# Kernel tuning notes

Measured on AMD Instinct MI355X. Metric: run time of the kernel, lower is better.

## Reference

```python
import jax, jax.numpy as jnp
import numpy as np
import math

EMB_DIM = 1024
N_HEADS = 16
HEAD_DIM = EMB_DIM // N_HEADS
B, T = 4, 2048


def bitlinear(x, w):
    # BitNet b1.58 absmean ternary quantization. NOTE: the source never
    # rescales the ternary weights by `scale`, so forward uses raw {-1,0,1}.
    scale = jnp.maximum(jnp.mean(jnp.abs(w)), 1e-8)
    w_ternary = jnp.clip(jnp.round(w / scale), -1.0, 1.0)
    w_q = w + jax.lax.stop_gradient(w_ternary - w)  # STE
    return x @ w_q.T


def setup_inputs() -> dict:
    key = jax.random.key(0)
    k1, k2, k3 = jax.random.split(key, 3)
    x = jax.random.normal(k1, (B, T, EMB_DIM), dtype=jnp.float32)
    w_qkv = jax.random.normal(k2, (3 * EMB_DIM, EMB_DIM), dtype=jnp.float32) * 0.02
    w_out = jax.random.normal(k3, (EMB_DIM, EMB_DIM), dtype=jnp.float32) * 0.02
    return {"x": x, "w_qkv": w_qkv, "w_out": w_out}


def reference(x, w_qkv, w_out):
    Bc, Tc, C = x.shape
    qkv = bitlinear(x, w_qkv)  # [B, T, 3C]
    q, k, v = jnp.split(qkv, 3, axis=2)

    def split_heads(t):  # [B, T, C] -> [B, H, T, D]
        return t.reshape(Bc, Tc, N_HEADS, HEAD_DIM).transpose(0, 2, 1, 3)

    q, k, v = split_heads(q), split_heads(k), split_heads(v)
    scale = math.sqrt(HEAD_DIM)
    scores = jnp.einsum("bhqd,bhkd->bhqk", q, k) / scale  # [B, H, T, T]
    causal = jnp.triu(jnp.ones((Tc, Tc), dtype=bool), k=1)
    scores = jnp.where(causal, -jnp.inf, scores)
    attn = jax.nn.softmax(scores, axis=-1)
    out = jnp.einsum("bhqk,bhkd->bhqd", attn, v)  # [B, H, T, D]
    out = out.transpose(0, 2, 1, 3).reshape(Bc, Tc, C)
    return bitlinear(out, w_out)
```

## Files before the change

kernel.cpp:

```cpp
#include <hip/hip_runtime.h>
#include <hip/hip_bf16.h>

#define EMB   1024
#define NHEAD 16
#define HDIM  64
#define BSZ   4
#define SEQ   2048
#define MROWS (BSZ*SEQ)
#define NQKV  (3*EMB)

typedef __bf16 bf16;
typedef __bf16 bf16v8 __attribute__((ext_vector_type(8)));
typedef float  f32v4  __attribute__((ext_vector_type(4)));
typedef int    i32v4  __attribute__((ext_vector_type(4)));

#define MFMA16(a,b,c)  __builtin_amdgcn_mfma_f32_16x16x32_bf16((a),(b),(c),0,0,0)
#define MFMAI8(a,b,c)  __builtin_amdgcn_mfma_i32_16x16x64_i8((a),(b),(c),0,0,0)

__device__ __forceinline__ void gload_lds16(const void* g, void* l) {
  __builtin_amdgcn_global_load_lds((const __attribute__((address_space(1))) void*)g,
                                   (__attribute__((address_space(3))) void*)l,
                                   16, 0, 0);
}


__global__ void zero2_kernel(float* p) { p[threadIdx.x] = 0.f; }

__global__ void abs_sum_kernel(const float* __restrict__ w, int n, float* out) {
  float s = 0.f;
  for (int i = blockIdx.x * blockDim.x + threadIdx.x; i < n; i += gridDim.x * blockDim.x)
    s += fabsf(w[i]);
  #pragma unroll
  for (int off = 32; off; off >>= 1) s += __shfl_down(s, off, 64);
  __shared__ float red[4];
  int lane = threadIdx.x & 63, wid = threadIdx.x >> 6;
  if (lane == 0) red[wid] = s;
  __syncthreads();
  if (threadIdx.x == 0) atomicAdd(out, red[0] + red[1] + red[2] + red[3]);
}

__global__ void ternarize_i8_kernel(const float* __restrict__ w, int n,
                                    const float* __restrict__ sum, char* __restrict__ out) {
  int i = blockIdx.x * blockDim.x + threadIdx.x;
  if (i >= n) return;
  float scale = fmaxf(*sum / (float)n, 1e-8f);
  float t = rintf(w[i] / scale);
  t = fmaxf(-1.f, fminf(1.f, t));
  out[i] = (char)(int)t;
}

__global__ void ternarize_bf16_kernel(const float* __restrict__ w, int n,
                                      const float* __restrict__ sum, bf16* __restrict__ out) {
  int i = blockIdx.x * blockDim.x + threadIdx.x;
  if (i >= n) return;
  float scale = fmaxf(*sum / (float)n, 1e-8f);
  float t = rintf(w[i] / scale);
  t = fmaxf(-1.f, fminf(1.f, t));
  out[i] = (bf16)t;
}

__global__ void quant_x_kernel(const float* __restrict__ x, char* __restrict__ p1,
                               char* __restrict__ p2, int n) {
  int i = blockIdx.x * blockDim.x + threadIdx.x;
  if (i >= n) return;
  float v = x[i];
  float q1 = fminf(fmaxf(rintf(v * 16.f), -127.f), 127.f);
  float r = v - q1 * 0.0625f;
  float q2 = fminf(fmaxf(rintf(r * 4096.f), -127.f), 127.f);
  p1[i] = (char)(int)q1;
  p2[i] = (char)(int)q2;
}


__launch_bounds__(256, 2)
__global__ void gemm_qkv_kernel(const char* __restrict__ xq1, const char* __restrict__ xq2,
                                const char* __restrict__ w8,
                                bf16* __restrict__ qh, bf16* __restrict__ ql,
                                bf16* __restrict__ kh, bf16* __restrict__ kl,
                                bf16* __restrict__ vv) {
  __shared__ __align__(16) char A1[128 * 64];
  __shared__ __align__(16) char A2[128 * 64];
  __shared__ __align__(16) char Bs[128 * 64];
  const int tid = threadIdx.x;
  const int lane = tid & 63, wid = tid >> 6;
  const int quad = lane >> 4, l16 = lane & 15;
  const int m0 = blockIdx.x * 128, n0 = blockIdx.y * 128;
  const int wm = (wid >> 1) * 64, wn = (wid & 1) * 64;
  const int asw = (l16 >> 1) & 3;
  i32v4 acc1[4][4] = {};
  i32v4 acc2[4][4] = {};

  for (int kt = 0; kt < EMB / 64; ++kt) {
    __syncthreads();
    #pragma unroll
    for (int r = 0; r < 2; ++r) {
      int li = r * 256 + tid;
      int row = li >> 2, cs = li & 3;
      int cg = cs ^ ((row >> 1) & 3);
      gload_lds16(xq1 + (size_t)(m0 + row) * EMB + kt * 64 + cg * 16, &A1[li * 16]);
      gload_lds16(xq2 + (size_t)(m0 + row) * EMB + kt * 64 + cg * 16, &A2[li * 16]);
      gload_lds16(w8  + (size_t)(n0 + row) * EMB + kt * 64 + cg * 16, &Bs[li * 16]);
    }
    __syncthreads();
    i32v4 af1[4], af2[4], bfr[4];
    #pragma unroll
    for (int i = 0; i < 4; ++i) {
      int arow = wm + i * 16 + l16;
      int off = arow * 64 + ((quad ^ asw) * 16);
      af1[i] = *(const i32v4*)&A1[off];
      af2[i] = *(const i32v4*)&A2[off];
      int brow = wn + i * 16 + l16;
      bfr[i] = *(const i32v4*)&Bs[brow * 64 + ((quad ^ asw) * 16)];
    }
    #pragma unroll
    for (int i = 0; i < 4; ++i)
      #pragma unroll
      for (int j = 0; j < 4; ++j) {
        acc1[i][j] = MFMAI8(af1[i], bfr[j], acc1[i][j]);
        acc2[i][j] = MFMAI8(af2[i], bfr[j], acc2[i][j]);
      }
  }
  const float S1 = 0.0625f, S2 = 1.f / 4096.f;
  const float QSCALE = 0.18033688011112042f;
  #pragma unroll
  for (int i = 0; i < 4; ++i)
    #pragma unroll
    for (int j = 0; j < 4; ++j)
      #pragma unroll
      for (int r = 0; r < 4; ++r) {
        int m = m0 + wm + i * 16 + quad * 4 + r;
        int n = n0 + wn + j * 16 + l16;
        float c = (float)acc1[i][j][r] * S1 + (float)acc2[i][j][r] * S2;
        int b = m >> 11, t = m & (SEQ - 1);
        int region = n >> 10, c1 = n & 1023, h = c1 >> 6, d = c1 & 63;
        size_t idx = (((size_t)(b * NHEAD + h) * SEQ + t) << 6) + d;
        if (region == 0)      { float cs = c * QSCALE; bf16 hi = (bf16)cs; qh[idx] = hi; ql[idx] = (bf16)(cs - (float)hi); }
        else if (region == 1) { bf16 hi = (bf16)c; kh[idx] = hi; kl[idx] = (bf16)(c - (float)hi); }
        else                  { vv[idx] = (bf16)c; }
      }
}


__global__ void transpose_v_kernel(const bf16* __restrict__ v, bf16* __restrict__ vt) {
  __shared__ bf16 tile[64 * 72];
  const int tid = threadIdx.x;
  const int bh = blockIdx.y, t0 = blockIdx.x * 64;
  const size_t base = (size_t)bh * SEQ * HDIM;
  #pragma unroll
  for (int r = 0; r < 2; ++r) {
    int li = r * 256 + tid;
    int row = li >> 3, col = (li & 7) * 8;
    bf16v8 val = *(const bf16v8*)(v + base + (size_t)(t0 + row) * HDIM + col);
    #pragma unroll
    for (int j = 0; j < 8; ++j) tile[(col + j) * 72 + row] = val[j];
  }
  __syncthreads();
  #pragma unroll
  for (int r = 0; r < 2; ++r) {
    int li = r * 256 + tid;
    int drow = li >> 3, tcol = (li & 7) * 8;
    bf16v8 val;
    #pragma unroll
    for (int j = 0; j < 8; ++j) val[j] = tile[drow * 72 + tcol + j];
    *(bf16v8*)(vt + base + (size_t)drow * SEQ + t0 + tcol) = val;
  }
}


__launch_bounds__(512, 4)
__global__ void attn_kernel(const bf16* __restrict__ qh, const bf16* __restrict__ ql,
                            const bf16* __restrict__ kh, const bf16* __restrict__ kl,
                            const bf16* __restrict__ vt, bf16* __restrict__ o) {
  __shared__ __align__(16) char smem[66560];
  bf16* Qh = (bf16*)smem;
  bf16* Ql = (bf16*)(smem + 16384);
  bf16* Pw = (bf16*)(smem + 49152);
  const int tid = threadIdx.x;
  const int lane = tid & 63, wid = tid >> 6;
  const int quad = lane >> 4, l16 = lane & 15;
  const int xs = l16 & 7;
  const int pair = blockIdx.x;
  const int bh = blockIdx.y;
  const size_t base = (size_t)bh * SEQ * HDIM;

  const int srow = tid >> 3, scg = (tid & 7) ^ (srow & 7);
  auto stage_kv = [&](char* dst, int k0) {
    gload_lds16(kh + base + (size_t)(k0 + srow) * HDIM + scg * 8, (bf16*)dst + (size_t)tid * 8);
    gload_lds16(kl + base + (size_t)(k0 + srow) * HDIM + scg * 8, (bf16*)(dst + 8192) + (size_t)tid * 8);
    gload_lds16(vt + base + (size_t)srow * SEQ + k0 + scg * 8,    (bf16*)(dst + 16384) + (size_t)tid * 8);
  };

  bf16v8 ones_f;
  {
    bf16 v1 = (l16 == 0) ? (bf16)1.0f : (bf16)0.0f;
    #pragma unroll
    for (int j = 0; j < 8; ++j) ones_f[j] = v1;
  }
  const int b = bh >> 4, h = bh & 15;

  for (int phase = 0; phase < 2; ++phase) {
    const int qt = phase ? (7 - pair) : (8 + pair);
    const int q0 = qt * 128;

    __syncthreads();
    #pragma unroll
    for (int r = 0; r < 2; ++r) {
      int li = r * 512 + tid;
      int row = li >> 3, cg = (li & 7) ^ (row & 7);
      gload_lds16(qh + base + (size_t)(q0 + row) * HDIM + cg * 8, &Qh[li * 8]);
      gload_lds16(ql + base + (size_t)(q0 + row) * HDIM + cg * 8, &Ql[li * 8]);
    }
    __syncthreads();
    bf16v8 qhf[2], qlf[2];
    #pragma unroll
    for (int kk = 0; kk < 2; ++kk) {
      int off = (wid * 16 + l16) * 64 + (((kk << 2) | quad) ^ xs) * 8;
      qhf[kk] = *(const bf16v8*)&Qh[off];
      qlf[kk] = *(const bf16v8*)&Ql[off];
    }
    __syncthreads();

    f32v4 oacc[4] = {};
    f32v4 lacc = {};
    float mrow[4];
    #pragma unroll
    for (int r = 0; r < 4; ++r) mrow[r] = -1e30f;

    const int qrow_hi = q0 + wid * 16 + 15;
    const int ntiles = 2 * qt + 2;

    stage_kv(smem, 0);

    for (int ktile = 0; ktile < ntiles; ++ktile) {
      char* cb = smem + (size_t)((ktile & 1) * 24576);
      char* nb = smem + (size_t)(((ktile + 1) & 1) * 24576);
      __syncthreads();
      if (ktile + 1 < ntiles) stage_kv(nb, (ktile + 1) * 64);
      const int k0 = ktile * 64;
      if (k0 > qrow_hi) continue;

      bf16* Kh_ = (bf16*)cb;
      bf16* Kl_ = (bf16*)(cb + 8192);
      bf16* Vt_ = (bf16*)(cb + 16384);

      f32v4 sacc[4] = {};
      #pragma unroll
      for (int kk = 0; kk < 2; ++kk) {
        const int co = (((kk << 2) | quad) ^ xs) * 8;
        bf16v8 khf[4], klf[4];
        #pragma unroll
        for (int nt = 0; nt < 4; ++nt) {
          khf[nt] = *(const bf16v8*)&Kh_[(nt * 16 + l16) * 64 + co];
          klf[nt] = *(const bf16v8*)&Kl_[(nt * 16 + l16) * 64 + co];
        }
        #pragma unroll
        for (int nt = 0; nt < 4; ++nt) {
          sacc[nt] = MFMA16(qhf[kk], khf[nt], sacc[nt]);
          sacc[nt] = MFMA16(qhf[kk], klf[nt], sacc[nt]);
          sacc[nt] = MFMA16(qlf[kk], khf[nt], sacc[nt]);
        }
      }

      const int qrow_base = q0 + wid * 16 + quad * 4;
      #pragma unroll
      for (int nt = 0; nt < 4; ++nt) {
        int key = k0 + nt * 16 + l16;
        #pragma unroll
        for (int r = 0; r < 4; ++r)
          if (key > qrow_base + r) sacc[nt][r] = -1e30f;
      }
      float mnew[4], alpha[4];
      #pragma unroll
      for (int r = 0; r < 4; ++r) {
        float mx = fmaxf(fmaxf(sacc[0][r], sacc[1][r]), fmaxf(sacc[2][r], sacc[3][r]));
        #pragma unroll
        for (int off = 8; off; off >>= 1) mx = fmaxf(mx, __shfl_xor(mx, off, 64));
        mnew[r] = fmaxf(mrow[r], mx);
        alpha[r] = __builtin_amdgcn_exp2f(mrow[r] - mnew[r]);
        mrow[r] = mnew[r];
      }
      bf16* pwave = Pw + wid * (16 * 68);
      #pragma unroll
      for (int nt = 0; nt < 4; ++nt)
        #pragma unroll
        for (int r = 0; r < 4; ++r)
          pwave[(quad * 4 + r) * 68 + nt * 16 + l16] =
              (bf16)__builtin_amdgcn_exp2f(sacc[nt][r] - mnew[r]);
      #pragma unroll
      for (int r = 0; r < 4; ++r) {
        lacc[r] *= alpha[r];
        #pragma unroll
        for (int dt = 0; dt < 4; ++dt) oacc[dt][r] *= alpha[r];
      }

      #pragma unroll
      for (int kk = 0; kk < 2; ++kk) {
        bf16v8 pf = *(const bf16v8*)&pwave[l16 * 68 + kk * 32 + quad * 8];
        const int co = (((kk << 2) | quad) ^ xs) * 8;
        lacc = MFMA16(pf, ones_f, lacc);
        #pragma unroll
        for (int dt = 0; dt < 4; ++dt) {
          bf16v8 vf = *(const bf16v8*)&Vt_[(dt * 16 + l16) * 64 + co];
          oacc[dt] = MFMA16(pf, vf, oacc[dt]);
        }
      }
    }

    float lrow[4];
    #pragma unroll
    for (int r = 0; r < 4; ++r) lrow[r] = __shfl(lacc[r], lane & 48, 64);

    #pragma unroll
    for (int dt = 0; dt < 4; ++dt)
      #pragma unroll
      for (int r = 0; r < 4; ++r) {
        int q = q0 + wid * 16 + quad * 4 + r;
        int d = dt * 16 + l16;
        float val = oacc[dt][r] / lrow[r];
        o[((size_t)(b * SEQ + q)) * EMB + h * HDIM + d] = (bf16)val;
      }
  }
}


__launch_bounds__(256, 2)
__global__ void gemm_out_kernel(const bf16* __restrict__ oin, const bf16* __restrict__ wt,
                                float* __restrict__ out) {
  __shared__ __align__(16) bf16 As_[128 * 64];
  __shared__ __align__(16) bf16 Bs_[128 * 64];
  const int tid = threadIdx.x;
  const int lane = tid & 63, wid = tid >> 6;
  const int quad = lane >> 4, l16 = lane & 15;
  const int m0 = blockIdx.x * 128, n0 = blockIdx.y * 128;
  const int wm = (wid >> 1) * 64, wn = (wid & 1) * 64;
  f32v4 acc[4][4] = {};

  for (int kt = 0; kt < EMB / 64; ++kt) {
    __syncthreads();
    #pragma unroll
    for (int r = 0; r < 4; ++r) {
      int li = r * 256 + tid;
      int row = li >> 3, col = (li & 7) * 8;
      gload_lds16(oin + (size_t)(m0 + row) * EMB + kt * 64 + col, &As_[li * 8]);
      gload_lds16(wt  + (size_t)(n0 + row) * EMB + kt * 64 + col, &Bs_[li * 8]);
    }
    __syncthreads();
    #pragma unroll
    for (int kk = 0; kk < 2; ++kk) {
      bf16v8 af[4], bfr[4];
      #pragma unroll
      for (int i = 0; i < 4; ++i) {
        af[i]  = *(const bf16v8*)&As_[(wm + i * 16 + l16) * 64 + kk * 32 + quad * 8];
        bfr[i] = *(const bf16v8*)&Bs_[(wn + i * 16 + l16) * 64 + kk * 32 + quad * 8];
      }
      #pragma unroll
      for (int i = 0; i < 4; ++i)
        #pragma unroll
        for (int j = 0; j < 4; ++j)
          acc[i][j] = MFMA16(af[i], bfr[j], acc[i][j]);
    }
  }
  #pragma unroll
  for (int i = 0; i < 4; ++i)
    #pragma unroll
    for (int j = 0; j < 4; ++j)
      #pragma unroll
      for (int r = 0; r < 4; ++r) {
        int m = m0 + wm + i * 16 + quad * 4 + r;
        int n = n0 + wn + j * 16 + l16;
        out[(size_t)m * EMB + n] = acc[i][j][r];
      }
}


extern "C" void kernel_launch(void* const* d_in, const int* in_sizes, int n_in,
                              void* d_out, int out_size, void* d_ws, size_t ws_size,
                              hipStream_t stream) {
  const float* x     = (const float*)d_in[0];
  const float* w_qkv = (const float*)d_in[1];
  const float* w_out = (const float*)d_in[2];
  float* out = (float*)d_out;
  char* ws = (char*)d_ws;

  const size_t SZ  = (size_t)MROWS * EMB * sizeof(bf16);
  const size_t SZ8 = (size_t)MROWS * EMB;
  size_t off = 0;
  float* sums = (float*)ws;            off = 256;
  char*  wq8  = (char*)(ws + off);     off += (size_t)NQKV * EMB;
  bf16*  wo_t = (bf16*)(ws + off);     off += (size_t)EMB * EMB * sizeof(bf16);
  char*  xq1  = (char*)(ws + off);     off += SZ8;
  char*  xq2  = (char*)(ws + off);     off += SZ8;
  bf16*  qh   = (bf16*)(ws + off);     off += SZ;
  bf16*  ql   = (bf16*)(ws + off);     off += SZ;
  bf16*  kh   = (bf16*)(ws + off);     off += SZ;
  bf16*  kl   = (bf16*)(ws + off);     off += SZ;
  bf16*  vv   = (bf16*)(ws + off);     off += SZ;
  bf16*  vt   = (bf16*)xq1;
  bf16*  ob   = vv;
  (void)in_sizes; (void)n_in; (void)out_size; (void)ws_size;

  zero2_kernel<<<1, 2, 0, stream>>>(sums);
  abs_sum_kernel<<<256, 256, 0, stream>>>(w_qkv, NQKV * EMB, &sums[0]);
  abs_sum_kernel<<<256, 256, 0, stream>>>(w_out, EMB * EMB, &sums[1]);
  ternarize_i8_kernel<<<(NQKV * EMB) / 256, 256, 0, stream>>>(w_qkv, NQKV * EMB, &sums[0], wq8);
  ternarize_bf16_kernel<<<(EMB * EMB) / 256, 256, 0, stream>>>(w_out, EMB * EMB, &sums[1], wo_t);
  quant_x_kernel<<<(MROWS * EMB) / 256, 256, 0, stream>>>(x, xq1, xq2, MROWS * EMB);
  gemm_qkv_kernel<<<dim3(MROWS / 128, NQKV / 128), 256, 0, stream>>>(xq1, xq2, wq8, qh, ql, kh, kl, vv);
  transpose_v_kernel<<<dim3(SEQ / 64, BSZ * NHEAD), 256, 0, stream>>>(vv, vt);
  attn_kernel<<<dim3(8, BSZ * NHEAD), 512, 0, stream>>>(qh, ql, kh, kl, vt, ob);
  gemm_out_kernel<<<dim3(MROWS / 128, EMB / 128), 256, 0, stream>>>(ob, wo_t, out);
}
```

Before: 355.1 us.

## Give each attention wave 32 query rows to reuse K/V fragments

Attention blocks drop from 512 to 256 threads, and each wave now handles two 16-row query sub-tiles instead of one. K and V fragments loaded from LDS are therefore shared across twice as many MFMAs, halving LDS fragment reads per query row. The row-max reduction uses DPP row-shift ops instead of __shfl_xor. The costs are more registers per wave and fewer waves per block to hide latency. Some score MFMAs are also computed for fully masked sub-tiles.

```diff
diff --git a/kernel.cpp b/kernel.cpp
--- a/kernel.cpp
+++ b/kernel.cpp
@@ -22,6 +22,10 @@
                                    (__attribute__((address_space(3))) void*)l,
                                    16, 0, 0);
 }
+
+#define DPP_FMAX(x, ctrl) do {                                                     \
+    int _t = __builtin_amdgcn_update_dpp(0, __float_as_int(x), (ctrl), 0xf, 0xf, true); \
+    (x) = fmaxf((x), __int_as_float(_t)); } while (0)
 
 
 __global__ void zero2_kernel(float* p) { p[threadIdx.x] = 0.f; }
@@ -167,7 +171,7 @@
 }
 
 
-__launch_bounds__(512, 4)
+__launch_bounds__(256, 2)
 __global__ void attn_kernel(const bf16* __restrict__ qh, const bf16* __restrict__ ql,
                             const bf16* __restrict__ kh, const bf16* __restrict__ kl,
                             const bf16* __restrict__ vt, bf16* __restrict__ o) {
@@ -183,11 +187,15 @@
   const int bh = blockIdx.y;
   const size_t base = (size_t)bh * SEQ * HDIM;
 
-  const int srow = tid >> 3, scg = (tid & 7) ^ (srow & 7);
   auto stage_kv = [&](char* dst, int k0) {
-    gload_lds16(kh + base + (size_t)(k0 + srow) * HDIM + scg * 8, (bf16*)dst + (size_t)tid * 8);
-    gload_lds16(kl + base + (size_t)(k0 + srow) * HDIM + scg * 8, (bf16*)(dst + 8192) + (size_t)tid * 8);
-    gload_lds16(vt + base + (size_t)srow * SEQ + k0 + scg * 8,    (bf16*)(dst + 16384) + (size_t)tid * 8);
+    #pragma unroll
+    for (int r = 0; r < 2; ++r) {
+      int li = r * 256 + tid;
+      int srow = li >> 3, scg = (li & 7) ^ (srow & 7);
+      gload_lds16(kh + base + (size_t)(k0 + srow) * HDIM + scg * 8, (bf16*)dst + (size_t)li * 8);
+      gload_lds16(kl + base + (size_t)(k0 + srow) * HDIM + scg * 8, (bf16*)(dst + 8192) + (size_t)li * 8);
+      gload_lds16(vt + base + (size_t)srow * SEQ + k0 + scg * 8,    (bf16*)(dst + 16384) + (size_t)li * 8);
+    }
   };
 
   bf16v8 ones_f;
@@ -204,29 +212,34 @@
 
     __syncthreads();
     #pragma unroll
-    for (int r = 0; r < 2; ++r) {
-      int li = r * 512 + tid;
+    for (int r = 0; r < 4; ++r) {
+      int li = r * 256 + tid;
       int row = li >> 3, cg = (li & 7) ^ (row & 7);
       gload_lds16(qh + base + (size_t)(q0 + row) * HDIM + cg * 8, &Qh[li * 8]);
       gload_lds16(ql + base + (size_t)(q0 + row) * HDIM + cg * 8, &Ql[li * 8]);
     }
     __syncthreads();
-    bf16v8 qhf[2], qlf[2];
-    #pragma unroll
-    for (int kk = 0; kk < 2; ++kk) {
-      int off = (wid * 16 + l16) * 64 + (((kk << 2) | quad) ^ xs) * 8;
-      qhf[kk] = *(const bf16v8*)&Qh[off];
-      qlf[kk] = *(const bf16v8*)&Ql[off];
-    }
-    __syncthreads();
-
-    f32v4 oacc[4] = {};
-    f32v4 lacc = {};
-    float mrow[4];
-    #pragma unroll
-    for (int r = 0; r < 4; ++r) mrow[r] = -1e30f;
-
-    const int qrow_hi = q0 + wid * 16 + 15;
+    bf16v8 qhf[2][2], qlf[2][2];
+    #pragma unroll
+    for (int sub = 0; sub < 2; ++sub)
+      #pragma unroll
+      for (int kk = 0; kk < 2; ++kk) {
+        int off = (wid * 32 + sub * 16 + l16) * 64 + (((kk << 2) | quad) ^ xs) * 8;
+        qhf[sub][kk] = *(const bf16v8*)&Qh[off];
+        qlf[sub][kk] = *(const bf16v8*)&Ql[off];
+      }
+    __syncthreads();
+
+    f32v4 oacc[2][4] = {};
+    f32v4 lacc[2] = {};
+    float mrow[2][4];
+    #pragma unroll
+    for (int s = 0; s < 2; ++s)
+      #pragma unroll
+      for (int r = 0; r < 4; ++r) mrow[s][r] = -1e30f;
+
+    const int qw0 = q0 + wid * 32;
+    const int qrow_hi = qw0 + 31;
     const int ntiles = 2 * qt + 2;
 
     stage_kv(smem, 0);
@@ -243,7 +256,7 @@
       bf16* Kl_ = (bf16*)(cb + 8192);
       bf16* Vt_ = (bf16*)(cb + 16384);
 
-      f32v4 sacc[4] = {};
+      f32v4 sacc[2][4] = {};
       #pragma unroll
       for (int kk = 0; kk < 2; ++kk) {
         const int co = (((kk << 2) | quad) ^ xs) * 8;
@@ -254,71 +267,88 @@
           klf[nt] = *(const bf16v8*)&Kl_[(nt * 16 + l16) * 64 + co];
         }
         #pragma unroll
+        for (int sub = 0; sub < 2; ++sub)
+          #pragma unroll
+          for (int nt = 0; nt < 4; ++nt) {
+            sacc[sub][nt] = MFMA16(qhf[sub][kk], khf[nt], sacc[sub][nt]);
+            sacc[sub][nt] = MFMA16(qhf[sub][kk], klf[nt], sacc[sub][nt]);
+            sacc[sub][nt] = MFMA16(qlf[sub][kk], khf[nt], sacc[sub][nt]);
+          }
+      }
+
+      #pragma unroll
+      for (int sub = 0; sub < 2; ++sub) {
+        if (k0 > qw0 + sub * 16 + 15) continue;
+        const int qrow_base = qw0 + sub * 16 + quad * 4;
+        #pragma unroll
         for (int nt = 0; nt < 4; ++nt) {
-          sacc[nt] = MFMA16(qhf[kk], khf[nt], sacc[nt]);
-          sacc[nt] = MFMA16(qhf[kk], klf[nt], sacc[nt]);
-          sacc[nt] = MFMA16(qlf[kk], khf[nt], sacc[nt]);
-        }
-      }
-
-      const int qrow_base = q0 + wid * 16 + quad * 4;
-      #pragma unroll
-      for (int nt = 0; nt < 4; ++nt) {
-        int key = k0 + nt * 16 + l16;
-        #pragma unroll
-        for (int r = 0; r < 4; ++r)
-          if (key > qrow_base + r) sacc[nt][r] = -1e30f;
-      }
-      float mnew[4], alpha[4];
-      #pragma unroll
-      for (int r = 0; r < 4; ++r) {
-        float mx = fmaxf(fmaxf(sacc[0][r], sacc[1][r]), fmaxf(sacc[2][r], sacc[3][r]));
-        #pragma unroll
-        for (int off = 8; off; off >>= 1) mx = fmaxf(mx, __shfl_xor(mx, off, 64));
-        mnew[r] = fmaxf(mrow[r], mx);
-        alpha[r] = __builtin_amdgcn_exp2f(mrow[r] - mnew[r]);
-        mrow[r] = mnew[r];
-      }
-      bf16* pwave = Pw + wid * (16 * 68);
-      #pragma unroll
-      for (int nt = 0; nt < 4; ++nt)
-        #pragma unroll
-        for (int r = 0; r < 4; ++r)
-          pwave[(quad * 4 + r) * 68 + nt * 16 + l16] =
-              (bf16)__builtin_amdgcn_exp2f(sacc[nt][r] - mnew[r]);
-      #pragma unroll
-      for (int r = 0; r < 4; ++r) {
-        lacc[r] *= alpha[r];
-        #pragma unroll
-        for (int dt = 0; dt < 4; ++dt) oacc[dt][r] *= alpha[r];
+          int key = k0 + nt * 16 + l16;
+          #pragma unroll
+          for (int r = 0; r < 4; ++r)
+            if (key > qrow_base + r) sacc[sub][nt][r] = -1e30f;
+        }
+        float alpha[4];
+        #pragma unroll
+        for (int r = 0; r < 4; ++r) {
+          float mx = fmaxf(fmaxf(sacc[sub][0][r], sacc[sub][1][r]),
+                           fmaxf(sacc[sub][2][r], sacc[sub][3][r]));
+          DPP_FMAX(mx, 0x128);
+          DPP_FMAX(mx, 0x124);
+          DPP_FMAX(mx, 0x122);
+          DPP_FMAX(mx, 0x121);
+          float mnew = fmaxf(mrow[sub][r], mx);
+          alpha[r] = __builtin_amdgcn_exp2f(mrow[sub][r] - mnew);
+          mrow[sub][r] = mnew;
+        }
+        bf16* pwave = Pw + (wid * 2 + sub) * (16 * 68);
+        #pragma unroll
+        for (int nt = 0; nt < 4; ++nt)
+          #pragma unroll
+          for (int r = 0; r < 4; ++r)
+            pwave[(quad * 4 + r) * 68 + nt * 16 + l16] =
+                (bf16)__builtin_amdgcn_exp2f(sacc[sub][nt][r] - mrow[sub][r]);
+        #pragma unroll
+        for (int r = 0; r < 4; ++r) {
+          lacc[sub][r] *= alpha[r];
+          #pragma unroll
+          for (int dt = 0; dt < 4; ++dt) oacc[sub][dt][r] *= alpha[r];
+        }
       }
 
       #pragma unroll
       for (int kk = 0; kk < 2; ++kk) {
-        bf16v8 pf = *(const bf16v8*)&pwave[l16 * 68 + kk * 32 + quad * 8];
         const int co = (((kk << 2) | quad) ^ xs) * 8;
-        lacc = MFMA16(pf, ones_f, lacc);
-        #pragma unroll
-        for (int dt = 0; dt < 4; ++dt) {
-          bf16v8 vf = *(const bf16v8*)&Vt_[(dt * 16 + l16) * 64 + co];
-          oacc[dt] = MFMA16(pf, vf, oacc[dt]);
-        }
-      }
-    }
-
-    float lrow[4];
-    #pragma unroll
-    for (int r = 0; r < 4; ++r) lrow[r] = __shfl(lacc[r], lane & 48, 64);
-
-    #pragma unroll
-    for (int dt = 0; dt < 4; ++dt)
-      #pragma unroll
-      for (int r = 0; r < 4; ++r) {
-        int q = q0 + wid * 16 + quad * 4 + r;
-        int d = dt * 16 + l16;
-        float val = oacc[dt][r] / lrow[r];
-        o[((size_t)(b * SEQ + q)) * EMB + h * HDIM + d] = (bf16)val;
-      }
+        bf16v8 vf[4];
+        #pragma unroll
+        for (int dt = 0; dt < 4; ++dt)
+          vf[dt] = *(const bf16v8*)&Vt_[(dt * 16 + l16) * 64 + co];
+        #pragma unroll
+        for (int sub = 0; sub < 2; ++sub) {
+          if (k0 > qw0 + sub * 16 + 15) continue;
+          bf16v8 pf = *(const bf16v8*)&Pw[(wid * 2 + sub) * (16 * 68) + l16 * 68 + kk * 32 + quad * 8];
+          lacc[sub] = MFMA16(pf, ones_f, lacc[sub]);
+          #pragma unroll
+          for (int dt = 0; dt < 4; ++dt)
+            oacc[sub][dt] = MFMA16(pf, vf[dt], oacc[sub][dt]);
+        }
+      }
+    }
+
+    #pragma unroll
+    for (int sub = 0; sub < 2; ++sub) {
+      float lrow[4];
+      #pragma unroll
+      for (int r = 0; r < 4; ++r) lrow[r] = __shfl(lacc[sub][r], lane & 48, 64);
+      #pragma unroll
+      for (int dt = 0; dt < 4; ++dt)
+        #pragma unroll
+        for (int r = 0; r < 4; ++r) {
+          int q = q0 + wid * 32 + sub * 16 + quad * 4 + r;
+          int d = dt * 16 + l16;
+          float val = oacc[sub][dt][r] / lrow[r];
+          o[((size_t)(b * SEQ + q)) * EMB + h * HDIM + d] = (bf16)val;
+        }
+    }
   }
 }
 
@@ -407,6 +437,6 @@
   quant_x_kernel<<<(MROWS * EMB) / 256, 256, 0, stream>>>(x, xq1, xq2, MROWS * EMB);
   gemm_qkv_kernel<<<dim3(MROWS / 128, NQKV / 128), 256, 0, stream>>>(xq1, xq2, wq8, qh, ql, kh, kl, vv);
   transpose_v_kernel<<<dim3(SEQ / 64, BSZ * NHEAD), 256, 0, stream>>>(vv, vt);
-  attn_kernel<<<dim3(8, BSZ * NHEAD), 512, 0, stream>>>(qh, ql, kh, kl, vt, ob);
+  attn_kernel<<<dim3(8, BSZ * NHEAD), 256, 0, stream>>>(qh, ql, kh, kl, vt, ob);
   gemm_out_kernel<<<dim3(MROWS / 128, EMB / 128), 256, 0, stream>>>(ob, wo_t, out);
 }
```

Result: faster. 344.6 us (-3.0%).
